# Optimization experiments

Hardware: AMD Instinct MI355X
Metric: run time of the kernel (lower is better)

The kernel has to match this reference:

```python
import jax, jax.numpy as jnp
import numpy as np

B, T, D = 2, 4096, 1024      # batch, seq, hidden_dim
E, I = 16, 512               # n_routed_experts, expert_intermediate
K = 2                        # n_activated_experts
IS = 2048                    # shared_expert_intermediate
ALPHA = 1e-4                 # balance_loss_alpha
EPS = 1e-9


def setup_inputs() -> dict:
    key = jax.random.key(0)
    ks = jax.random.split(key, 8)
    s = lambda k, shape, fan: jax.random.normal(k, shape, jnp.float32) * (fan ** -0.5)
    return {
        "x": jax.random.normal(ks[0], (B, T, D), jnp.float32),
        "gate_w": s(ks[1], (D, E), D),            # router gate (no bias)
        "expert_bias": jnp.zeros((E,), jnp.float32),
        "sh_gate": s(ks[2], (D, IS), D),          # shared expert SwiGLU
        "sh_up": s(ks[3], (D, IS), D),
        "sh_down": s(ks[4], (IS, D), IS),
        "ex_gate": s(ks[5], (E, D, I), D),        # routed experts (stacked)
        "ex_up": s(ks[6], (E, D, I), D),
        "ex_down": s(ks[7], (E, I, D), I),
    }


def _swiglu(x, wg, wu, wd):
    return (jax.nn.silu(x @ wg) * (x @ wu)) @ wd


def reference(x, gate_w, expert_bias, sh_gate, sh_up, sh_down, ex_gate, ex_up, ex_down):
    Bq, Tq, Dq = x.shape
    # shared expert path (n_shared_experts = 1)
    shared = _swiglu(x, sh_gate, sh_up, sh_down)

    xf = x.reshape(Bq * Tq, Dq)                       # (N, D)
    N = xf.shape[0]

    # --- router: sigmoid gating, bias-adjusted top-k, normalized gates ---
    affinity = jax.nn.sigmoid(xf @ gate_w)            # (N, E)
    scores = affinity + expert_bias[None, :]
    _, idx = jax.lax.top_k(scores, K)                 # (N, K) int
    gv = jnp.take_along_axis(affinity, idx, axis=1)   # (N, K) gathered from affinity
    gv = gv / (gv.sum(-1, keepdims=True) + EPS)

    # --- balance loss (sequence-wise, Eq. 17-20) ---
    expert_mask = jax.nn.one_hot(idx, E, dtype=jnp.float32).sum(1)  # (N, E)
    f = expert_mask.sum(0) * E / (K * N)
    P = (affinity / (affinity.sum(-1, keepdims=True) + EPS)).mean(0)
    balance_loss = ALPHA * (f * P).sum()
    expert_counts = expert_mask.sum(0).astype(jnp.int32)            # (E,)

    # --- dispatch/compute/combine, expressed as dense combine-weight matrix ---
    # w[n, e] = sum of gate values for token n routed to expert e (same math
    # as the masked gather/scatter loop in the original)
    w = jnp.zeros((N, E), jnp.float32).at[jnp.arange(N)[:, None], idx].add(gv)
    h = jax.nn.silu(jnp.einsum('nd,edi->eni', xf, ex_gate)) \
        * jnp.einsum('nd,edi->eni', xf, ex_up)        # (E, N, I)
    routed = jnp.einsum('ne,eni,eid->nd', w, h, ex_down)  # (N, D)
    routed = routed.reshape(Bq, Tq, Dq)

    output = shared + routed  # note: original does NOT add residual despite docstring
    return output, balance_loss, expert_counts
```

## Files before the change

kernel.cpp:

```cpp
#include <hip/hip_runtime.h>
#include <stdint.h>

#define NTOK 8192
#define DDIM 1024
#define NEXP 16
#define KSEL 2
#define ISH 2048
#define IEX 512
#define ALPHAC 1e-4f
#define REPS 1e-9f

typedef __attribute__((ext_vector_type(8))) short short8;
typedef __attribute__((ext_vector_type(4))) float f32x4;

__device__ __forceinline__ unsigned short f2bf(float f){
  union { float f; uint32_t u; } v; v.f = f;
  uint32_t u = v.u;
  uint32_t r = (u + 0x7fffu + ((u >> 16) & 1u)) >> 16;
  return (unsigned short)r;
}
__device__ __forceinline__ float bf2f(unsigned short h){
  union { uint32_t u; float f; } v; v.u = ((uint32_t)h) << 16; return v.f;
}

__device__ __forceinline__ void gload16(const void* g, void* l){
  __builtin_amdgcn_global_load_lds(
      (const __attribute__((address_space(1))) void*)g,
      (__attribute__((address_space(3))) void*)l, 16, 0, 0);
}

__global__ __launch_bounds__(256) void convert_f32_bf16(const float* __restrict__ in,
                                                        unsigned short* __restrict__ out){
  int id = blockIdx.x * 256 + threadIdx.x;
  float4 v = ((const float4*)in)[id];
  ushort4 o;
  o.x = f2bf(v.x); o.y = f2bf(v.y); o.z = f2bf(v.z); o.w = f2bf(v.w);
  ((ushort4*)out)[id] = o;
}

template<int RM, int RO>
__global__ __launch_bounds__(256) void transpose_bf16(const float* __restrict__ in,
                                                      unsigned short* __restrict__ outp,
                                                      int R, int C){
  __shared__ float tile[64][65];
  const float* ip = in + (size_t)blockIdx.z * R * C;
  unsigned short* op = outp + (size_t)blockIdx.z * R * C * RM;
  int c0 = blockIdx.x * 64, r0 = blockIdx.y * 64;
  int t = threadIdx.x;
  int tr = t >> 4, tc = (t & 15) * 4;
  #pragma unroll
  for (int i = 0; i < 4; ++i){
    float4 v = *(const float4*)&ip[(size_t)(r0 + tr + i*16) * C + c0 + tc];
    tile[tr + i*16][tc+0] = v.x;
    tile[tr + i*16][tc+1] = v.y;
    tile[tr + i*16][tc+2] = v.z;
    tile[tr + i*16][tc+3] = v.w;
  }
  __syncthreads();
  #pragma unroll
  for (int i = 0; i < 4; ++i){
    int oc = tr + i*16;
    ushort4 w;
    w.x = f2bf(tile[tc+0][oc]);
    w.y = f2bf(tile[tc+1][oc]);
    w.z = f2bf(tile[tc+2][oc]);
    w.w = f2bf(tile[tc+3][oc]);
    *(ushort4*)&op[(size_t)((c0 + oc) * RM + RO) * R + r0 + tc] = w;
  }
}

__global__ __launch_bounds__(256) void logits_kernel(
    const float* __restrict__ x, const float* __restrict__ gw,
    float* __restrict__ logits)
{
  __shared__ float gws[16][1024];
  const int t = threadIdx.x;
  #pragma unroll
  for (int k = 0; k < 16; ++k){
    int idx = t + k * 256;
    float4 v = ((const float4*)gw)[idx];
    int d = idx >> 2, e0 = (idx & 3) * 4;
    gws[e0+0][d] = v.x;
    gws[e0+1][d] = v.y;
    gws[e0+2][d] = v.z;
    gws[e0+3][d] = v.w;
  }
  __syncthreads();
  const int lane = t & 63, w = t >> 6;
  const int nb = blockIdx.x * 16 + w * 4;
  for (int i = 0; i < 4; ++i){
    const int n = nb + i;
    const float4* xr = (const float4*)(x + (size_t)n * DDIM);
    float4 xv[4];
    #pragma unroll
    for (int k = 0; k < 4; ++k) xv[k] = xr[lane + k*64];
    float acc[16];
    #pragma unroll
    for (int e = 0; e < 16; ++e){
      float s = 0.f;
      #pragma unroll
      for (int k = 0; k < 4; ++k){
        float4 g = *(const float4*)&gws[e][(lane + k*64)*4];
        s = fmaf(xv[k].x, g.x, fmaf(xv[k].y, g.y, fmaf(xv[k].z, g.z, fmaf(xv[k].w, g.w, s))));
      }
      acc[e] = s;
    }
    #pragma unroll
    for (int m = 1; m < 64; m <<= 1)
      #pragma unroll
      for (int e = 0; e < 16; ++e)
        acc[e] += __shfl_xor(acc[e], m);
    if (lane == 0){
      float4* op = (float4*)(logits + (size_t)n * 16);
      op[0] = make_float4(acc[0],  acc[1],  acc[2],  acc[3]);
      op[1] = make_float4(acc[4],  acc[5],  acc[6],  acc[7]);
      op[2] = make_float4(acc[8],  acc[9],  acc[10], acc[11]);
      op[3] = make_float4(acc[12], acc[13], acc[14], acc[15]);
    }
  }
}

__global__ __launch_bounds__(256) void router_finish(
    const float* __restrict__ logits, const float* __restrict__ ebias,
    int* __restrict__ idxb, float* __restrict__ gvb,
    float* __restrict__ Ppart, int* __restrict__ Cpart)
{
  __shared__ float Ps[16];
  __shared__ int Cs[16];
  const int t = threadIdx.x;
  if (t < 16){ Ps[t] = 0.f; Cs[t] = 0; }
  __syncthreads();
  const int lane = t & 63;
  const int n = blockIdx.x * 256 + t;
  const float4* lp = (const float4*)(logits + (size_t)n * 16);
  float4 a0 = lp[0], a1 = lp[1], a2 = lp[2], a3 = lp[3];
  float aff[16];
  aff[0]=a0.x; aff[1]=a0.y; aff[2]=a0.z; aff[3]=a0.w;
  aff[4]=a1.x; aff[5]=a1.y; aff[6]=a1.z; aff[7]=a1.w;
  aff[8]=a2.x; aff[9]=a2.y; aff[10]=a2.z; aff[11]=a2.w;
  aff[12]=a3.x; aff[13]=a3.y; aff[14]=a3.z; aff[15]=a3.w;
  float rowsum = REPS;
  #pragma unroll
  for (int e = 0; e < 16; ++e){
    aff[e] = 1.f / (1.f + __expf(-aff[e]));
    rowsum += aff[e];
  }
  float bj[16];
  #pragma unroll
  for (int e = 0; e < 16; ++e) bj[e] = ebias[e];
  float bestS = aff[0] + bj[0], bestA = aff[0]; int i1 = 0;
  #pragma unroll
  for (int j = 1; j < 16; ++j){
    float sc = aff[j] + bj[j];
    bool gt2 = sc > bestS;
    bestS = gt2 ? sc : bestS; bestA = gt2 ? aff[j] : bestA; i1 = gt2 ? j : i1;
  }
  float secS = -1e30f, secA = 0.f; int i2 = 0;
  #pragma unroll
  for (int j = 0; j < 16; ++j){
    float sc = aff[j] + bj[j];
    bool ok = (j != i1) && (sc > secS);
    secS = ok ? sc : secS; secA = ok ? aff[j] : secA; i2 = ok ? j : i2;
  }
  float den = bestA + secA + REPS;
  idxb[n*2]   = i1; idxb[n*2+1] = i2;
  gvb[n*2]    = bestA / den; gvb[n*2+1] = secA / den;

  float inv = 1.f / rowsum;
  float pv[16]; int cv[16];
  #pragma unroll
  for (int e = 0; e < 16; ++e){
    pv[e] = aff[e] * inv;
    cv[e] = (e == i1) + (e == i2);
  }
  #pragma unroll
  for (int m = 1; m < 64; m <<= 1)
    #pragma unroll
    for (int e = 0; e < 16; ++e){
      pv[e] += __shfl_xor(pv[e], m);
      cv[e] += __shfl_xor(cv[e], m);
    }
  if (lane == 0){
    #pragma unroll
    for (int e = 0; e < 16; ++e){
      atomicAdd(&Ps[e], pv[e]);
      atomicAdd(&Cs[e], cv[e]);
    }
  }
  __syncthreads();
  if (t < 16){ Ppart[blockIdx.x*16 + t] = Ps[t]; Cpart[blockIdx.x*16 + t] = Cs[t]; }
}

__global__ __launch_bounds__(256) void finalize2(
    const float* __restrict__ Ppart, const int* __restrict__ Cpart,
    int* __restrict__ counts, int* __restrict__ offs, int* __restrict__ cursor,
    float* __restrict__ out_tail)
{
  __shared__ float P[16];
  __shared__ int C[16];
  int t = threadIdx.x;
  if (t < 16){ P[t] = 0.f; C[t] = 0; }
  __syncthreads();
  if (t < 32){
    int e = t & 15, c = t >> 4;
    float p = 0.f; int cc = 0;
    for (int b = c * 16; b < c * 16 + 16; ++b){ p += Ppart[b*16 + e]; cc += Cpart[b*16 + e]; }
    atomicAdd(&P[e], p); atomicAdd(&C[e], cc);
  }
  __syncthreads();
  if (t == 0){
    int a = 0; float loss = 0.f;
    for (int i = 0; i < 16; ++i){
      offs[i] = a; cursor[i] = a; counts[i] = C[i]; a += C[i];
      loss += ((float)C[i] * (float)NEXP / (float)(KSEL * NTOK)) * (P[i] / (float)NTOK);
      out_tail[1+i] = (float)C[i];
    }
    out_tail[0] = ALPHAC * loss;
  }
}

__global__ __launch_bounds__(256) void slot_assign(
    const int* __restrict__ idxb, const float* __restrict__ gvb,
    int* __restrict__ cursor, int* __restrict__ tokp, float* __restrict__ gatep,
    int* __restrict__ rslot)
{
  int i = blockIdx.x * 256 + threadIdx.x;
  int e = idxb[i];
  int s = atomicAdd(&cursor[e], 1);
  tokp[s] = i >> 1;
  gatep[s] = gvb[i];
  rslot[i] = s;
}

template<bool GROUPED, bool GATHER, int MODE, int NYT>
__global__ __launch_bounds__(256) void gemm128(
    const unsigned short* __restrict__ A,
    const unsigned short* __restrict__ B,
    void* __restrict__ Cout,
    int M, int N, int K,
    const int* __restrict__ counts,
    const int* __restrict__ offsets,
    const int* __restrict__ perm,
    const float* __restrict__ rowscale)
{
  __shared__ __align__(16) unsigned short As[128*64];
  __shared__ __align__(16) unsigned short Bs[128*64];

  const int nwg = gridDim.x;
  const int bid = blockIdx.x;
  const int wg = (bid & 7) * (nwg >> 3) + (bid >> 3);
  const int mtl = wg / NYT;
  const int nt  = wg % NYT;

  int mt = mtl, off = 0, cnt = M;
  const unsigned short* bp = B;
  if (GROUPED){
    int acc_ = 0, e = -1;
    #pragma unroll
    for (int i = 0; i < NEXP; ++i){
      int c = counts[i]; int tt = (c + 127) >> 7;
      if (e < 0 && mtl < acc_ + tt){ e = i; mt = mtl - acc_; off = offsets[i]; cnt = c; }
      acc_ += tt;
    }
    if (e < 0) return;
    bp += (size_t)e * N * K;
  }
  const int m0 = mt * 128, n0 = nt * 128;
  const int t = threadIdx.x;
  const int lane = t & 63;
  const int wid = t >> 6;
  const int wm = (wid >> 1) * 64;
  const int wn = (wid & 1) * 64;
  const int l15 = lane & 15, g = lane >> 4;

  const unsigned short* asrc[4];
  const unsigned short* bsrc[4];
  int ldso[4];
  #pragma unroll
  for (int c = 0; c < 4; ++c){
    int s = (wid*4 + c)*64 + lane;
    int row = s >> 3, c16 = s & 7;
    int scol = (c16 ^ (row & 7)) * 8;
    ldso[c] = (wid*4 + c) * 512;
    int r = m0 + row;
    int rc = GROUPED ? (r < cnt ? r : (cnt > 0 ? cnt - 1 : 0)) : r;
    int ar;
    if (GATHER) ar = perm[off + rc];
    else        ar = GROUPED ? off + rc : rc;
    asrc[c] = A + (size_t)ar * K + scol;
    bsrc[c] = bp + (size_t)(n0 + row) * K + scol;
  }

  f32x4 acc[4][4];
  #pragma unroll
  for (int i = 0; i < 4; ++i)
    #pragma unroll
    for (int j = 0; j < 4; ++j)
      #pragma unroll
      for (int r = 0; r < 4; ++r) acc[i][j][r] = 0.f;

  const int ntk = K >> 6;
  for (int tk = 0; tk < ntk; ++tk){
    const int k0 = tk << 6;
    #pragma unroll
    for (int c = 0; c < 4; ++c) gload16(asrc[c] + k0, (void*)&As[ldso[c]]);
    #pragma unroll
    for (int c = 0; c < 4; ++c) gload16(bsrc[c] + k0, (void*)&Bs[ldso[c]]);
    __syncthreads();
    #pragma unroll
    for (int ks = 0; ks < 2; ++ks){
      short8 af[4], bf[4];
      #pragma unroll
      for (int i = 0; i < 4; ++i){
        int row = wm + i * 16 + l15;
        af[i] = *(const short8*)&As[row * 64 + (((ks*4 + g) ^ (row & 7)) * 8)];
      }
      #pragma unroll
      for (int j = 0; j < 4; ++j){
        int row = wn + j * 16 + l15;
        bf[j] = *(const short8*)&Bs[row * 64 + (((ks*4 + g) ^ (row & 7)) * 8)];
      }
      #pragma unroll
      for (int i = 0; i < 4; ++i)
        #pragma unroll
        for (int j = 0; j < 4; ++j)
          acc[i][j] = __builtin_amdgcn_mfma_f32_16x16x32_bf16(af[i], bf[j], acc[i][j], 0, 0, 0);
    }
    __syncthreads();
  }

  #pragma unroll
  for (int i = 0; i < 4; ++i)
    #pragma unroll
    for (int j = 0; j < 4; ++j)
      #pragma unroll
      for (int r = 0; r < 4; ++r){
        int lr = wm + i * 16 + g * 4 + r;
        int grow = m0 + lr;
        if (GROUPED && grow >= cnt) continue;
        int gcol = n0 + wn + j * 16 + l15;
        size_t orow = GROUPED ? (size_t)(off + grow) : (size_t)grow;
        float val = acc[i][j][r];
        if (MODE == 1){
          ((float*)Cout)[orow * N + gcol] = val;
        } else if (MODE == 6){
          float uo = __shfl_xor(val, 1);
          if (!(l15 & 1)){
            float rv = val / (1.f + __expf(-val)) * uo;
            ((unsigned short*)Cout)[orow * (N >> 1) + (gcol >> 1)] = f2bf(rv);
          }
        } else {
          val *= rowscale[off + grow];
          ((unsigned short*)Cout)[orow * N + gcol] = f2bf(val);
        }
      }
}

template<int MODE, int NYT>
__global__ __launch_bounds__(512, 1) void gemm256(
    const unsigned short* __restrict__ A,
    const unsigned short* __restrict__ B,
    void* __restrict__ Cout,
    int M, int N, int K)
{
  __shared__ __align__(16) unsigned short As[2][256*64];
  __shared__ __align__(16) unsigned short Bs[2][256*64];

  const int nwg = gridDim.x;
  const int bid = blockIdx.x;
  const int wg = (bid & 7) * (nwg >> 3) + (bid >> 3);
  const int mt  = wg / NYT;
  const int ntc = wg % NYT;

  const int m0 = mt * 256, n0 = ntc * 256;
  const int t = threadIdx.x;
  const int lane = t & 63;
  const int wid = t >> 6;
  const int wm0 = (wid >> 2) * 128;
  const int wn0 = (wid & 3) * 64;
  const int l15 = lane & 15, g = lane >> 4;

  const unsigned short* asrc[4];
  const unsigned short* bsrc[4];
  int ldst[4];
  #pragma unroll
  for (int c = 0; c < 4; ++c){
    int slot = c * 512 + t;
    int row = slot >> 3, c16 = slot & 7;
    int scol = (c16 ^ (row & 7)) * 8;
    ldst[c] = slot * 8;
    asrc[c] = A + (size_t)(m0 + row) * K + scol;
    bsrc[c] = B + (size_t)(n0 + row) * K + scol;
  }

  f32x4 acc[8][4];
  #pragma unroll
  for (int i = 0; i < 8; ++i)
    #pragma unroll
    for (int j = 0; j < 4; ++j)
      #pragma unroll
      for (int r = 0; r < 4; ++r) acc[i][j][r] = 0.f;

  auto STAGE = [&](int buf, int kt){
    const int k0 = kt << 6;
    #pragma unroll
    for (int c = 0; c < 4; ++c) gload16(asrc[c] + k0, (void*)&As[buf][ldst[c]]);
    #pragma unroll
    for (int c = 0; c < 4; ++c) gload16(bsrc[c] + k0, (void*)&Bs[buf][ldst[c]]);
  };

  const int ntk = K >> 6;
  STAGE(0, 0);
  __syncthreads();
  int cur = 0;
  for (int tk = 0; tk < ntk; ++tk){
    if (tk + 1 < ntk) STAGE(cur ^ 1, tk + 1);
    short8 bfr[4][2];
    #pragma unroll
    for (int j = 0; j < 4; ++j)
      #pragma unroll
      for (int ks = 0; ks < 2; ++ks){
        int row = wn0 + j * 16 + l15;
        bfr[j][ks] = *(const short8*)&Bs[cur][row * 64 + (((ks*4 + g) ^ (row & 7)) * 8)];
      }
    #pragma unroll
    for (int mi = 0; mi < 8; ++mi){
      int row = wm0 + mi * 16 + l15;
      short8 af0 = *(const short8*)&As[cur][row * 64 + (((0 + g) ^ (row & 7)) * 8)];
      short8 af1 = *(const short8*)&As[cur][row * 64 + (((4 + g) ^ (row & 7)) * 8)];
      #pragma unroll
      for (int j = 0; j < 4; ++j)
        acc[mi][j] = __builtin_amdgcn_mfma_f32_16x16x32_bf16(af0, bfr[j][0], acc[mi][j], 0, 0, 0);
      #pragma unroll
      for (int j = 0; j < 4; ++j)
        acc[mi][j] = __builtin_amdgcn_mfma_f32_16x16x32_bf16(af1, bfr[j][1], acc[mi][j], 0, 0, 0);
    }
    __syncthreads();
    cur ^= 1;
  }

  #pragma unroll
  for (int mi = 0; mi < 8; ++mi)
    #pragma unroll
    for (int j = 0; j < 4; ++j)
      #pragma unroll
      for (int r = 0; r < 4; ++r){
        int lr = wm0 + mi * 16 + g * 4 + r;
        int grow = m0 + lr;
        int gcol = n0 + wn0 + j * 16 + l15;
        float val = acc[mi][j][r];
        if (MODE == 6){
          float uo = __shfl_xor(val, 1);
          if (!(l15 & 1)){
            float rv = val / (1.f + __expf(-val)) * uo;
            ((unsigned short*)Cout)[(size_t)grow * (N >> 1) + (gcol >> 1)] = f2bf(rv);
          }
        } else {
          ((float*)Cout)[(size_t)grow * N + gcol] = val;
        }
      }
}

__global__ __launch_bounds__(256) void combine_kernel(float* __restrict__ out,
                                                      const unsigned short* __restrict__ ybuf,
                                                      const int* __restrict__ rs){
  int id = blockIdx.x * 256 + threadIdx.x;
  int n = id >> 8;
  int q = id & 255;
  int s0 = rs[n*2], s1 = rs[n*2+1];
  float4 o = ((float4*)out)[id];
  ushort4 a = ((const ushort4*)(ybuf + (size_t)s0 * DDIM))[q];
  ushort4 b = ((const ushort4*)(ybuf + (size_t)s1 * DDIM))[q];
  o.x += bf2f(a.x) + bf2f(b.x);
  o.y += bf2f(a.y) + bf2f(b.y);
  o.z += bf2f(a.z) + bf2f(b.z);
  o.w += bf2f(a.w) + bf2f(b.w);
  ((float4*)out)[id] = o;
}

extern "C" void kernel_launch(void* const* d_in, const int* in_sizes, int n_in,
                              void* d_out, int out_size, void* d_ws, size_t ws_size,
                              hipStream_t stream)
{
  const float* x       = (const float*)d_in[0];
  const float* gate_w  = (const float*)d_in[1];
  const float* ebias   = (const float*)d_in[2];
  const float* sh_gate = (const float*)d_in[3];
  const float* sh_up   = (const float*)d_in[4];
  const float* sh_down = (const float*)d_in[5];
  const float* ex_gate = (const float*)d_in[6];
  const float* ex_up   = (const float*)d_in[7];
  const float* ex_down = (const float*)d_in[8];
  float* out = (float*)d_out;
  (void)in_sizes; (void)n_in; (void)out_size; (void)ws_size;

  size_t o = 0;
  auto alloc = [&](size_t bytes) -> void* {
    o = (o + 255) & ~(size_t)255;
    void* p = (char*)d_ws + o;
    o += bytes;
    return p;
  };
  unsigned short* xb    = (unsigned short*)alloc((size_t)NTOK*DDIM*2);
  unsigned short* shguT = (unsigned short*)alloc((size_t)2*ISH*DDIM*2);
  unsigned short* shdT  = (unsigned short*)alloc((size_t)DDIM*ISH*2);
  unsigned short* exguT = (unsigned short*)alloc((size_t)NEXP*2*IEX*DDIM*2);
  unsigned short* exdT  = (unsigned short*)alloc((size_t)NEXP*DDIM*IEX*2);
  unsigned short* hbuf  = (unsigned short*)alloc((size_t)NTOK*KSEL*IEX*2);
  unsigned short* big   = (unsigned short*)alloc((size_t)NTOK*ISH*2);
  float* logits = (float*)alloc((size_t)NTOK*NEXP*4);
  int*   idxb  = (int*)alloc(NTOK*KSEL*4);
  float* gvb   = (float*)alloc(NTOK*KSEL*4);
  float* Ppart = (float*)alloc(32*16*4);
  int*   Cpart = (int*)alloc(32*16*4);
  int*   counts= (int*)alloc(64);
  int*   offs  = (int*)alloc(64);
  int*   cursor= (int*)alloc(64);
  int*   tokp  = (int*)alloc(NTOK*KSEL*4);
  float* gatep = (float*)alloc(NTOK*KSEL*4);
  int*   rslot = (int*)alloc(NTOK*KSEL*4);

  convert_f32_bf16<<<NTOK*DDIM/1024, 256, 0, stream>>>(x, xb);
  transpose_bf16<2,0><<<dim3(ISH/64,  DDIM/64, 1),    256, 0, stream>>>(sh_gate, shguT, DDIM, ISH);
  transpose_bf16<2,1><<<dim3(ISH/64,  DDIM/64, 1),    256, 0, stream>>>(sh_up,   shguT, DDIM, ISH);
  transpose_bf16<1,0><<<dim3(DDIM/64, ISH/64,  1),    256, 0, stream>>>(sh_down, shdT, ISH, DDIM);
  transpose_bf16<2,0><<<dim3(IEX/64,  DDIM/64, NEXP), 256, 0, stream>>>(ex_gate, exguT, DDIM, IEX);
  transpose_bf16<2,1><<<dim3(IEX/64,  DDIM/64, NEXP), 256, 0, stream>>>(ex_up,   exguT, DDIM, IEX);
  transpose_bf16<1,0><<<dim3(DDIM/64, IEX/64,  NEXP), 256, 0, stream>>>(ex_down, exdT, IEX, DDIM);

  logits_kernel<<<512, 256, 0, stream>>>(x, gate_w, logits);
  router_finish<<<32, 256, 0, stream>>>(logits, ebias, idxb, gvb, Ppart, Cpart);
  finalize2<<<1, 256, 0, stream>>>(Ppart, Cpart, counts, offs, cursor,
                                   out + (size_t)NTOK*DDIM);
  slot_assign<<<NTOK*KSEL/256, 256, 0, stream>>>(idxb, gvb, cursor, tokp, gatep, rslot);

  gemm256<6,16><<<32*16, 512, 0, stream>>>(
      xb, shguT, big, NTOK, 2*ISH, DDIM);
  gemm128<false,false,1,8><<<64*8, 256, 0, stream>>>(
      big, shdT, out, NTOK, DDIM, ISH, nullptr, nullptr, nullptr, nullptr);

  gemm128<true,true,6,8><<<144*8, 256, 0, stream>>>(
      xb, exguT, hbuf, 0, 2*IEX, DDIM, counts, offs, tokp, nullptr);
  gemm128<true,false,2,8><<<144*8, 256, 0, stream>>>(
      hbuf, exdT, big, 0, DDIM, IEX, counts, offs, nullptr, gatep);

  combine_kernel<<<NTOK*DDIM/1024, 256, 0, stream>>>(out, big, rslot);
}
```

Before: 398.3 us.

## Fuse bf16 x conversion into router logits and scatter-add expert outputs directly

The fp32-to-bf16 conversion of x now happens inside the router logits kernel, which already reads x, so a separate pass over the input is removed. The expert down-projection GEMM now scales by the gate and atomically adds its fp32 results straight into the output rows of each token. This drops the bf16 staging buffer, the slot index array and the combine kernel. In exchange it relies on float atomics to global memory, which make the summation order nondeterministic and may contend when two experts hit the same token row.

```diff
diff --git a/kernel.cpp b/kernel.cpp
--- a/kernel.cpp
+++ b/kernel.cpp
@@ -27,15 +27,6 @@
   __builtin_amdgcn_global_load_lds(
       (const __attribute__((address_space(1))) void*)g,
       (__attribute__((address_space(3))) void*)l, 16, 0, 0);
-}
-
-__global__ __launch_bounds__(256) void convert_f32_bf16(const float* __restrict__ in,
-                                                        unsigned short* __restrict__ out){
-  int id = blockIdx.x * 256 + threadIdx.x;
-  float4 v = ((const float4*)in)[id];
-  ushort4 o;
-  o.x = f2bf(v.x); o.y = f2bf(v.y); o.z = f2bf(v.z); o.w = f2bf(v.w);
-  ((ushort4*)out)[id] = o;
 }
 
 template<int RM, int RO>
@@ -71,7 +62,7 @@
 
 __global__ __launch_bounds__(256) void logits_kernel(
     const float* __restrict__ x, const float* __restrict__ gw,
-    float* __restrict__ logits)
+    float* __restrict__ logits, unsigned short* __restrict__ xb)
 {
   __shared__ float gws[16][1024];
   const int t = threadIdx.x;
@@ -91,9 +82,17 @@
   for (int i = 0; i < 4; ++i){
     const int n = nb + i;
     const float4* xr = (const float4*)(x + (size_t)n * DDIM);
+    ushort4* xo = (ushort4*)(xb + (size_t)n * DDIM);
     float4 xv[4];
     #pragma unroll
     for (int k = 0; k < 4; ++k) xv[k] = xr[lane + k*64];
+    #pragma unroll
+    for (int k = 0; k < 4; ++k){
+      ushort4 ob;
+      ob.x = f2bf(xv[k].x); ob.y = f2bf(xv[k].y);
+      ob.z = f2bf(xv[k].z); ob.w = f2bf(xv[k].w);
+      xo[lane + k*64] = ob;
+    }
     float acc[16];
     #pragma unroll
     for (int e = 0; e < 16; ++e){
@@ -221,15 +220,13 @@
 
 __global__ __launch_bounds__(256) void slot_assign(
     const int* __restrict__ idxb, const float* __restrict__ gvb,
-    int* __restrict__ cursor, int* __restrict__ tokp, float* __restrict__ gatep,
-    int* __restrict__ rslot)
+    int* __restrict__ cursor, int* __restrict__ tokp, float* __restrict__ gatep)
 {
   int i = blockIdx.x * 256 + threadIdx.x;
   int e = idxb[i];
   int s = atomicAdd(&cursor[e], 1);
   tokp[s] = i >> 1;
   gatep[s] = gvb[i];
-  rslot[i] = s;
 }
 
 template<bool GROUPED, bool GATHER, int MODE, int NYT>
@@ -343,15 +340,16 @@
         float val = acc[i][j][r];
         if (MODE == 1){
           ((float*)Cout)[orow * N + gcol] = val;
+        } else if (MODE == 3){
+          val *= rowscale[off + grow];
+          int tok = perm[off + grow];
+          atomicAdd(&((float*)Cout)[(size_t)tok * N + gcol], val);
         } else if (MODE == 6){
           float uo = __shfl_xor(val, 1);
           if (!(l15 & 1)){
             float rv = val / (1.f + __expf(-val)) * uo;
             ((unsigned short*)Cout)[orow * (N >> 1) + (gcol >> 1)] = f2bf(rv);
           }
-        } else {
-          val *= rowscale[off + grow];
-          ((unsigned short*)Cout)[orow * N + gcol] = f2bf(val);
         }
       }
 }
@@ -459,23 +457,6 @@
           ((float*)Cout)[(size_t)grow * N + gcol] = val;
         }
       }
-}
-
-__global__ __launch_bounds__(256) void combine_kernel(float* __restrict__ out,
-                                                      const unsigned short* __restrict__ ybuf,
-                                                      const int* __restrict__ rs){
-  int id = blockIdx.x * 256 + threadIdx.x;
-  int n = id >> 8;
-  int q = id & 255;
-  int s0 = rs[n*2], s1 = rs[n*2+1];
-  float4 o = ((float4*)out)[id];
-  ushort4 a = ((const ushort4*)(ybuf + (size_t)s0 * DDIM))[q];
-  ushort4 b = ((const ushort4*)(ybuf + (size_t)s1 * DDIM))[q];
-  o.x += bf2f(a.x) + bf2f(b.x);
-  o.y += bf2f(a.y) + bf2f(b.y);
-  o.z += bf2f(a.z) + bf2f(b.z);
-  o.w += bf2f(a.w) + bf2f(b.w);
-  ((float4*)out)[id] = o;
 }
 
 extern "C" void kernel_launch(void* const* d_in, const int* in_sizes, int n_in,
@@ -518,9 +499,7 @@
   int*   cursor= (int*)alloc(64);
   int*   tokp  = (int*)alloc(NTOK*KSEL*4);
   float* gatep = (float*)alloc(NTOK*KSEL*4);
-  int*   rslot = (int*)alloc(NTOK*KSEL*4);
-
-  convert_f32_bf16<<<NTOK*DDIM/1024, 256, 0, stream>>>(x, xb);
+
   transpose_bf16<2,0><<<dim3(ISH/64,  DDIM/64, 1),    256, 0, stream>>>(sh_gate, shguT, DDIM, ISH);
   transpose_bf16<2,1><<<dim3(ISH/64,  DDIM/64, 1),    256, 0, stream>>>(sh_up,   shguT, DDIM, ISH);
   transpose_bf16<1,0><<<dim3(DDIM/64, ISH/64,  1),    256, 0, stream>>>(sh_down, shdT, ISH, DDIM);
@@ -528,11 +507,11 @@
   transpose_bf16<2,1><<<dim3(IEX/64,  DDIM/64, NEXP), 256, 0, stream>>>(ex_up,   exguT, DDIM, IEX);
   transpose_bf16<1,0><<<dim3(DDIM/64, IEX/64,  NEXP), 256, 0, stream>>>(ex_down, exdT, IEX, DDIM);
 
-  logits_kernel<<<512, 256, 0, stream>>>(x, gate_w, logits);
+  logits_kernel<<<512, 256, 0, stream>>>(x, gate_w, logits, xb);
   router_finish<<<32, 256, 0, stream>>>(logits, ebias, idxb, gvb, Ppart, Cpart);
   finalize2<<<1, 256, 0, stream>>>(Ppart, Cpart, counts, offs, cursor,
                                    out + (size_t)NTOK*DDIM);
-  slot_assign<<<NTOK*KSEL/256, 256, 0, stream>>>(idxb, gvb, cursor, tokp, gatep, rslot);
+  slot_assign<<<NTOK*KSEL/256, 256, 0, stream>>>(idxb, gvb, cursor, tokp, gatep);
 
   gemm256<6,16><<<32*16, 512, 0, stream>>>(
       xb, shguT, big, NTOK, 2*ISH, DDIM);
@@ -541,8 +520,6 @@
 
   gemm128<true,true,6,8><<<144*8, 256, 0, stream>>>(
       xb, exguT, hbuf, 0, 2*IEX, DDIM, counts, offs, tokp, nullptr);
-  gemm128<true,false,2,8><<<144*8, 256, 0, stream>>>(
-      hbuf, exdT, big, 0, DDIM, IEX, counts, offs, nullptr, gatep);
-
-  combine_kernel<<<NTOK*DDIM/1024, 256, 0, stream>>>(out, big, rslot);
-}
+  gemm128<true,false,3,8><<<144*8, 256, 0, stream>>>(
+      hbuf, exdT, out, 0, DDIM, IEX, counts, offs, tokp, gatep);
+}
```

Measured after the change: 416.2 us. 1.04x slower.
